# Kernel tuning notes

Hardware: AMD Instinct MI355X
Metric: run time of the kernel (lower is better)

Reference implementation:

```python
import jax, jax.numpy as jnp
import numpy as np

B, N, D, H = 16, 1024, 384, 6
DH = D // H  # 64 per-head dim


def _layernorm(x, w, b, eps=1e-5):
    mu = jnp.mean(x, axis=-1, keepdims=True)
    var = jnp.var(x, axis=-1, keepdims=True)
    return (x - mu) * jax.lax.rsqrt(var + eps) * w + b


def setup_inputs() -> dict:
    key = jax.random.key(0)
    ks = jax.random.split(key, 10)
    std = 0.02
    return {
        "X": jax.random.normal(ks[0], (B, N, D), dtype=jnp.float32),
        "Wq": jax.random.normal(ks[1], (H, DH, D), dtype=jnp.float32) * std,
        "Wk": jax.random.normal(ks[2], (H, DH, D), dtype=jnp.float32) * std,
        "Wv": jax.random.normal(ks[3], (H, DH, D), dtype=jnp.float32) * std,
        "Wo": jax.random.normal(ks[4], (D, D), dtype=jnp.float32) * std,
        "bo": jnp.zeros((D,), dtype=jnp.float32),
        "ln1_w": jnp.ones((D,), dtype=jnp.float32),
        "ln1_b": jnp.zeros((D,), dtype=jnp.float32),
        "ln2_w": jnp.ones((D,), dtype=jnp.float32),
        "ln2_b": jnp.zeros((D,), dtype=jnp.float32),
        "W1": jax.random.normal(ks[5], (2 * D, D), dtype=jnp.float32) * std,
        "b1": jnp.zeros((2 * D,), dtype=jnp.float32),
        "W2": jax.random.normal(ks[6], (D, 2 * D), dtype=jnp.float32) * std,
        "b2": jnp.zeros((D,), dtype=jnp.float32),
    }


def reference(X, Wq, Wk, Wv, Wo, bo, ln1_w, ln1_b, ln2_w, ln2_b, W1, b1, W2, b2):
    scale = 1.0 / jnp.sqrt(jnp.float32(DH))
    # pre-LN then multi-head attention (heads vectorized, math identical to per-head loop)
    t = _layernorm(X, ln1_w, ln1_b)                       # [B,N,D]
    q = jnp.einsum('bnd,hkd->bhnk', t, Wq)                # [B,H,N,DH]
    k = jnp.einsum('bnd,hkd->bhnk', t, Wk)
    v = jnp.einsum('bnd,hkd->bhnk', t, Wv)
    scores = jnp.einsum('bhnk,bhmk->bhnm', q, k) * scale  # [B,H,N,N]
    p = jax.nn.softmax(scores, axis=-1)
    o = jnp.einsum('bhnm,bhmk->bhnk', p, v)               # [B,H,N,DH]
    o = jnp.transpose(o, (0, 2, 1, 3)).reshape(B, N, D)   # concat heads
    attn = o @ Wo.T + bo
    # residual + post-LN (dropout/drop_path are identity in eval)
    X2 = _layernorm(X + attn, ln2_w, ln2_b)
    # MLP: Linear -> exact GELU -> Linear
    h = jax.nn.gelu(X2 @ W1.T + b1, approximate=False)
    mlp = h @ W2.T + b2
    return X2 + mlp
```

## Files before the change

### kernel.cpp

```cpp
#include <hip/hip_runtime.h>
#include <math.h>

typedef float  f32x4  __attribute__((ext_vector_type(4)));
typedef __bf16 bf16x8 __attribute__((ext_vector_type(8)));
typedef __bf16 bf16x4 __attribute__((ext_vector_type(4)));

__device__ __forceinline__ void gload16(const void* g, void* l) {
  __builtin_amdgcn_global_load_lds((__attribute__((address_space(1))) const void*)g,
                                   (__attribute__((address_space(3))) void*)l, 16, 0, 0);
}

__device__ __forceinline__ f32x4 mfma16(bf16x8 a, bf16x8 b, f32x4 c) {
  return __builtin_amdgcn_mfma_f32_16x16x32_bf16(a, b, c, 0, 0, 0);
}

__device__ __forceinline__ f32x4 mfma8(long a, long b, f32x4 c) {
  return __builtin_amdgcn_mfma_f32_16x16x32_fp8_fp8(a, b, c, 0, 0, 0);
}

__device__ __forceinline__ unsigned char f2fp8(float x) {
  return (unsigned char)__builtin_amdgcn_cvt_pk_fp8_f32(x, x, 0, false);
}

__device__ __forceinline__ float fast_gelu(float x) {
  const float xs = x * 0.70710678118654752f;
  const float ax = fabsf(xs);
  const float t  = __builtin_amdgcn_rcpf(1.f + 0.3275911f * ax);
  const float poly = ((((1.061405429f*t - 1.453152027f)*t + 1.421413741f)*t
                       - 0.284496736f)*t + 0.254829592f)*t;
  const float e = __builtin_amdgcn_exp2f(-1.4426950408889634f * ax * ax);
  float erfv = 1.f - poly * e;
  erfv = (xs < 0.f) ? -erfv : erfv;
  return 0.5f * x * (1.f + erfv);
}

__global__ __launch_bounds__(256) void prep_kernel(
    const float* __restrict__ X, const float* __restrict__ ln1w, const float* __restrict__ ln1b,
    unsigned char* __restrict__ t8,
    const float* __restrict__ Wq, const float* __restrict__ Wk, const float* __restrict__ Wv,
    const float* __restrict__ Wo, const float* __restrict__ W1, const float* __restrict__ W2,
    unsigned char* __restrict__ wqkv8, unsigned char* __restrict__ wo8,
    unsigned char* __restrict__ w18, unsigned char* __restrict__ w28)
{
  if (blockIdx.x >= 4096) {
    const int idx = ((blockIdx.x - 4096) * 256 + threadIdx.x) * 4;
    const float* src; unsigned char* dst; int off;
    if      (idx < 147456) { src = Wq; dst = wqkv8;          off = idx; }
    else if (idx < 294912) { src = Wk; dst = wqkv8 + 147456; off = idx - 147456; }
    else if (idx < 442368) { src = Wv; dst = wqkv8 + 294912; off = idx - 294912; }
    else if (idx < 589824) { src = Wo; dst = wo8;            off = idx - 442368; }
    else if (idx < 884736) { src = W1; dst = w18;            off = idx - 589824; }
    else                   { src = W2; dst = w28;            off = idx - 884736; }
    f32x4 v = *(const f32x4*)(src + off);
    int p = __builtin_amdgcn_cvt_pk_fp8_f32(v.x, v.y, 0, false);
    p     = __builtin_amdgcn_cvt_pk_fp8_f32(v.z, v.w, p, true);
    *(int*)(dst + off) = p;
    return;
  }
  const int row  = blockIdx.x * 4 + (threadIdx.x >> 6);
  const int lane = threadIdx.x & 63;
  const float* x = X + (size_t)row * 384;
  float v[6]; float s = 0.f;
#pragma unroll
  for (int j = 0; j < 6; ++j) { v[j] = x[lane + 64*j]; s += v[j]; }
#pragma unroll
  for (int off = 32; off > 0; off >>= 1) s += __shfl_xor(s, off);
  const float mu = s * (1.f/384.f);
  float s2 = 0.f;
#pragma unroll
  for (int j = 0; j < 6; ++j) { float d = v[j] - mu; s2 += d*d; }
#pragma unroll
  for (int off = 32; off > 0; off >>= 1) s2 += __shfl_xor(s2, off);
  const float inv = rsqrtf(s2 * (1.f/384.f) + 1e-5f);
#pragma unroll
  for (int j = 0; j < 6; ++j) {
    const int cidx = lane + 64*j;
    t8[(size_t)row*384 + cidx] = f2fp8((v[j]-mu)*inv*ln1w[cidx] + ln1b[cidx]);
  }
}

__global__ __launch_bounds__(256) void ln_kernel(
    const float* __restrict__ in, const float* __restrict__ w, const float* __restrict__ b,
    unsigned char* __restrict__ outc, float* __restrict__ outf)
{
  const int row  = blockIdx.x * 4 + (threadIdx.x >> 6);
  const int lane = threadIdx.x & 63;
  const float* x = in + (size_t)row * 384;
  float v[6]; float s = 0.f;
#pragma unroll
  for (int j = 0; j < 6; ++j) { v[j] = x[lane + 64*j]; s += v[j]; }
#pragma unroll
  for (int off = 32; off > 0; off >>= 1) s += __shfl_xor(s, off);
  const float mu = s * (1.f/384.f);
  float s2 = 0.f;
#pragma unroll
  for (int j = 0; j < 6; ++j) { float d = v[j] - mu; s2 += d*d; }
#pragma unroll
  for (int off = 32; off > 0; off >>= 1) s2 += __shfl_xor(s2, off);
  const float inv = rsqrtf(s2 * (1.f/384.f) + 1e-5f);
#pragma unroll
  for (int j = 0; j < 6; ++j) {
    const int cidx = lane + 64*j;
    const float y = (v[j]-mu)*inv*w[cidx] + b[cidx];
    outc[(size_t)row*384 + cidx] = f2fp8(y);
    outf[(size_t)row*384 + cidx] = y;
  }
}

template<int EPI>
__global__ __launch_bounds__(256, 3) void gemm_f8(
    const unsigned char* __restrict__ A, const unsigned char* __restrict__ Bw,
    int N, int K,
    const float* __restrict__ bias, const float* __restrict__ resid,
    float* __restrict__ outf, unsigned char* __restrict__ outc,
    __bf16* __restrict__ q_out, __bf16* __restrict__ k_out, __bf16* __restrict__ vt_out)
{
  __shared__ __attribute__((aligned(16))) unsigned char As[2][8192];
  __shared__ __attribute__((aligned(16))) unsigned char Bs[2][8192];
  const int tid  = threadIdx.x;
  const int lane = tid & 63;
  const int w    = tid >> 6;
  const int wm   = w >> 1, wn = w & 1;
  const int m0   = blockIdx.x * 128, n0 = blockIdx.y * 128;

  f32x4 acc[4][4] = {};

  const int srow = lane & 15, skq = (lane >> 4) << 4;
  const unsigned char* gptr[4];
  unsigned char*       lptr[4];
#pragma unroll
  for (int r = 0; r < 4; ++r) {
    const int id = r * 4 + w;
    if (id < 8) { gptr[r] = A  + (size_t)(m0 + id*16 + srow) * K + skq; lptr[r] = &As[0][id * 1024]; }
    else        { const int j = id - 8;
                  gptr[r] = Bw + (size_t)(n0 + j*16 + srow) * K + skq; lptr[r] = &Bs[0][j * 1024]; }
  }

  auto stage = [&](int kk, int b) {
#pragma unroll
    for (int r = 0; r < 4; ++r)
      gload16(gptr[r] + kk * 64, lptr[r] + b * 8192);
  };
  const int lo = lane & 15, quad = lane >> 4;
  const int foff = (quad >> 1) * 256 + lo * 16 + (quad & 1) * 8;
  auto compute = [&](int b) {
#pragma unroll
    for (int s = 0; s < 2; ++s) {
      long af[4], bfr[4];
#pragma unroll
      for (int i = 0; i < 4; ++i)
        af[i]  = *(const long*)&As[b][(wm*4 + i) * 1024 + s * 512 + foff];
#pragma unroll
      for (int j = 0; j < 4; ++j)
        bfr[j] = *(const long*)&Bs[b][(wn*4 + j) * 1024 + s * 512 + foff];
#pragma unroll
      for (int i = 0; i < 4; ++i)
#pragma unroll
        for (int j = 0; j < 4; ++j)
          acc[i][j] = mfma8(af[i], bfr[j], acc[i][j]);
    }
  };

  const int NIT = K >> 6;
  stage(0, 0);
  __syncthreads();
  for (int k = 0; k < NIT; ++k) {
    const int b = k & 1;
    if (k + 1 < NIT) stage(k + 1, b ^ 1);
    compute(b);
    __syncthreads();
  }

#pragma unroll
  for (int rt = 0; rt < 4; ++rt) {
#pragma unroll
    for (int ct = 0; ct < 4; ++ct) {
      const int gr0 = m0 + (wm*4 + rt)*16 + quad*4;
      const int gc  = n0 + (wn*4 + ct)*16 + lo;
      f32x4 a = acc[rt][ct];
      if constexpr (EPI == 0) {
        const int bb = gr0 >> 10, nn = gr0 & 1023;
        if (gc >= 768) {
          const int jj = gc - 768, hh = jj >> 6, dh = jj & 63;
          bf16x4 pk = {(__bf16)a[0], (__bf16)a[1], (__bf16)a[2], (__bf16)a[3]};
          *(bf16x4*)&vt_out[((size_t)((bb*6 + hh)*64 + dh) << 10) + nn] = pk;
        } else {
          const bool isq = (gc < 384);
          const int jj = isq ? gc : (gc - 384);
          __bf16* dst = isq ? q_out : k_out;
          const float sc = isq ? 0.18033688011112042f : 1.0f;
          const int hh = jj >> 6, dh = jj & 63;
#pragma unroll
          for (int i = 0; i < 4; ++i)
            dst[((size_t)(((bb*6 + hh) << 10) | (nn + i)) << 6) + dh] = (__bf16)(a[i] * sc);
        }
      } else {
#pragma unroll
        for (int i = 0; i < 4; ++i) {
          const int gr = gr0 + i;
          float val = a[i];
          if constexpr (EPI == 1) {
            const size_t idx = (size_t)gr * N + gc;
            outf[idx] = val + bias[gc] + resid[idx];
          } else if constexpr (EPI == 2) {
            outc[(size_t)gr * N + gc] = f2fp8(fast_gelu(val + bias[gc]));
          } else {
            const size_t idx = (size_t)gr * N + gc;
            outf[idx] = outf[idx] + val + bias[gc];
          }
        }
      }
    }
  }
}

__global__ __launch_bounds__(256, 3) void attn_kernel(
    const __bf16* __restrict__ qp, const __bf16* __restrict__ kp,
    const __bf16* __restrict__ vtp, unsigned char* __restrict__ omat8)
{
  __shared__ __attribute__((aligned(16))) __bf16 Ks[3][4096];
  __shared__ __attribute__((aligned(16))) __bf16 Vs[2][4096];
  __shared__ __attribute__((aligned(16))) __bf16 Ps[4][1088];
  const int tid = threadIdx.x, lane = tid & 63, w = tid >> 6;
  const int bh = blockIdx.x;
  const int q0 = blockIdx.y * 128 + w * 32;
  const int quad = lane >> 4, lo = lane & 15;

  bf16x8 qa[2][2];
#pragma unroll
  for (int t = 0; t < 2; ++t) {
    const __bf16* qb = qp + ((size_t)bh * 1024 + q0 + t*16 + lo) * 64 + (quad << 3);
    qa[t][0] = *(const bf16x8*)qb;
    qa[t][1] = *(const bf16x8*)(qb + 32);
  }

  f32x4 oacc[2][4] = {};
  float l_r[2] = {0.f, 0.f};

  auto stageK = [&](int c, int kb) {
#pragma unroll
    for (int s = 0; s < 2; ++s) {
      const int ck = s * 256 + tid;
      const int l = ck & 63, g = ck >> 6;
      const int ct = g >> 1, ks = g & 1;
      const __bf16* gk = kp + ((size_t)bh*1024 + c*64 + ct*16 + (l & 15)) * 64
                            + ks*32 + ((l >> 4) << 3);
      gload16(gk, &Ks[kb][(ck & ~63) * 8]);
    }
  };
  auto stageV = [&](int c, int vb) {
#pragma unroll
    for (int s = 0; s < 2; ++s) {
      const int ck = s * 256 + tid;
      const int l = ck & 63, g = ck >> 6;
      const int ct = g >> 1, ks = g & 1;
      const __bf16* gv = vtp + (((size_t)(bh*64 + ct*16 + (l & 15))) << 10)
                             + c*64 + ks*32 + ((l >> 4) << 3);
      gload16(gv, &Vs[vb][(ck & ~63) * 8]);
    }
  };

  stageK(0, 0); stageK(1, 1); stageV(0, 0);
  asm volatile("s_waitcnt vmcnt(0)" ::: "memory");
  __builtin_amdgcn_s_barrier();

  for (int c = 0; c < 16; ++c) {
    const int kb = c % 3;
    const int vb = c & 1;
    if (c + 2 < 16) stageK(c + 2, (c + 2) % 3);
    if (c + 1 < 16) stageV(c + 1, (c + 1) & 1);

    f32x4 st[2][4];
#pragma unroll
    for (int ct = 0; ct < 4; ++ct) {
      bf16x8 kb0 = *(const bf16x8*)&Ks[kb][((ct*2 + 0)*64 + lane) * 8];
      bf16x8 kb1 = *(const bf16x8*)&Ks[kb][((ct*2 + 1)*64 + lane) * 8];
#pragma unroll
      for (int t = 0; t < 2; ++t) {
        f32x4 s0 = {};
        s0 = mfma16(kb0, qa[t][0], s0);
        s0 = mfma16(kb1, qa[t][1], s0);
        st[t][ct] = s0;
      }
    }
    bf16x8 pa[2][2];
#pragma unroll
    for (int t = 0; t < 2; ++t) {
#pragma unroll
      for (int ct = 0; ct < 4; ++ct) {
        const float p0 = __builtin_amdgcn_exp2f(st[t][ct][0]);
        const float p1 = __builtin_amdgcn_exp2f(st[t][ct][1]);
        const float p2 = __builtin_amdgcn_exp2f(st[t][ct][2]);
        const float p3 = __builtin_amdgcn_exp2f(st[t][ct][3]);
        l_r[t] += (p0 + p1) + (p2 + p3);
        bf16x4 pk = {(__bf16)p0, (__bf16)p1, (__bf16)p2, (__bf16)p3};
        *(bf16x4*)&Ps[w][lo*68 + ct*16 + quad*4] = pk;
      }
#pragma unroll
      for (int ks = 0; ks < 2; ++ks)
        pa[t][ks] = *(const bf16x8*)&Ps[w][lo*68 + ks*32 + (quad << 3)];
    }

    if (c <= 13)      asm volatile("s_waitcnt vmcnt(4)" ::: "memory");
    else if (c == 14) asm volatile("s_waitcnt vmcnt(2)" ::: "memory");
    else              asm volatile("s_waitcnt vmcnt(0)" ::: "memory");
    __builtin_amdgcn_sched_barrier(0);
    __builtin_amdgcn_s_barrier();

#pragma unroll
    for (int dt = 0; dt < 4; ++dt)
#pragma unroll
      for (int ks = 0; ks < 2; ++ks) {
        bf16x8 vbv = *(const bf16x8*)&Vs[vb][((dt*2 + ks)*64 + lane) * 8];
#pragma unroll
        for (int t = 0; t < 2; ++t)
          oacc[t][dt] = mfma16(pa[t][ks], vbv, oacc[t][dt]);
      }

    __builtin_amdgcn_s_barrier();
  }

  const int b = bh / 6, h = bh - (bh / 6) * 6;
#pragma unroll
  for (int t = 0; t < 2; ++t) {
    float ls = l_r[t];
    ls += __shfl_xor(ls, 16);
    ls += __shfl_xor(ls, 32);
#pragma unroll
    for (int i = 0; i < 4; ++i) {
      const float linv = 1.f / __shfl(ls, quad*4 + i);
      const int n = q0 + t*16 + quad*4 + i;
#pragma unroll
      for (int dt = 0; dt < 4; ++dt)
        omat8[((size_t)((b << 10) | n)) * 384 + (h << 6) + dt*16 + lo] =
            f2fp8(oacc[t][dt][i] * linv);
    }
  }
}

extern "C" void kernel_launch(void* const* d_in, const int* in_sizes, int n_in,
                              void* d_out, int out_size, void* d_ws, size_t ws_size,
                              hipStream_t stream)
{
  const float* X    = (const float*)d_in[0];
  const float* Wq   = (const float*)d_in[1];
  const float* Wk   = (const float*)d_in[2];
  const float* Wv   = (const float*)d_in[3];
  const float* Wo   = (const float*)d_in[4];
  const float* bo   = (const float*)d_in[5];
  const float* ln1w = (const float*)d_in[6];
  const float* ln1b = (const float*)d_in[7];
  const float* ln2w = (const float*)d_in[8];
  const float* ln2b = (const float*)d_in[9];
  const float* W1   = (const float*)d_in[10];
  const float* b1   = (const float*)d_in[11];
  const float* W2   = (const float*)d_in[12];
  const float* b2   = (const float*)d_in[13];

  char* ws = (char*)d_ws;
  unsigned char* t8   = (unsigned char*)(ws + 0);
  unsigned char* x2_f8 = (unsigned char*)(ws + 6291456);
  __bf16* q_bf  = (__bf16*)(ws + 12582912);
  __bf16* k_bf  = (__bf16*)(ws + 25165824);
  unsigned char* omat8 = (unsigned char*)(ws + 37748736);
  __bf16* vt_bf = (__bf16*)(ws + 50331648);
  float*  s1    = (float*) (ws + 62914560);
  unsigned char* h8 = (unsigned char*)(ws + 62914560);
  unsigned char* wqkv8 = (unsigned char*)(ws + 88080384);
  unsigned char* wo8 = (unsigned char*)(ws + 88522752);
  unsigned char* w18 = (unsigned char*)(ws + 88670208);
  unsigned char* w28 = (unsigned char*)(ws + 88965120);
  float*  out   = (float*)d_out;

  prep_kernel<<<5248, 256, 0, stream>>>(X, ln1w, ln1b, t8,
      Wq, Wk, Wv, Wo, W1, W2, wqkv8, wo8, w18, w28);
  gemm_f8<0><<<dim3(128,9), 256, 0, stream>>>(t8, wqkv8, 1152, 384,
      nullptr, nullptr, nullptr, nullptr, q_bf, k_bf, vt_bf);
  attn_kernel<<<dim3(96,8), 256, 0, stream>>>(q_bf, k_bf, vt_bf, omat8);
  gemm_f8<1><<<dim3(128,3), 256, 0, stream>>>(omat8, wo8, 384, 384,
      bo, X, s1, nullptr, nullptr, nullptr, nullptr);
  ln_kernel<<<4096, 256, 0, stream>>>(s1, ln2w, ln2b, x2_f8, out);
  gemm_f8<2><<<dim3(128,6), 256, 0, stream>>>(x2_f8, w18, 768, 384,
      b1, nullptr, nullptr, h8, nullptr, nullptr, nullptr);
  gemm_f8<3><<<dim3(128,3), 256, 0, stream>>>(h8, w28, 384, 768,
      b2, nullptr, out, nullptr, nullptr, nullptr, nullptr);
}
```

Before: 238.4 us.

## Load V tiles straight into registers and drop the V LDS buffer

The attention kernel no longer stages V chunks through a double-buffered LDS array. Each wave now loads its V fragments directly from global memory into registers, issued right after the score MFMAs and before the next K prefetch. This removes the mid-iteration barrier and its explicit vmcnt waits, and frees LDS so the launch bound can rise from 3 to 4 blocks per CU. The cost is that all four waves in a block fetch the same V tile, which multiplies global/L2 traffic for V. It also leans on in-order vmcnt completion and the end-of-iteration barrier to keep the K buffer reads safe.

```diff
diff --git a/kernel.cpp b/kernel.cpp
--- a/kernel.cpp
+++ b/kernel.cpp
@@ -214,12 +214,11 @@
   }
 }
 
-__global__ __launch_bounds__(256, 3) void attn_kernel(
+__global__ __launch_bounds__(256, 4) void attn_kernel(
     const __bf16* __restrict__ qp, const __bf16* __restrict__ kp,
     const __bf16* __restrict__ vtp, unsigned char* __restrict__ omat8)
 {
   __shared__ __attribute__((aligned(16))) __bf16 Ks[3][4096];
-  __shared__ __attribute__((aligned(16))) __bf16 Vs[2][4096];
   __shared__ __attribute__((aligned(16))) __bf16 Ps[4][1088];
   const int tid = threadIdx.x, lane = tid & 63, w = tid >> 6;
   const int bh = blockIdx.x;
@@ -237,7 +236,7 @@
   f32x4 oacc[2][4] = {};
   float l_r[2] = {0.f, 0.f};
 
-  auto stageK = [&](int c, int kb) {
+  auto stageK = [&](int c, int b) {
 #pragma unroll
     for (int s = 0; s < 2; ++s) {
       const int ck = s * 256 + tid;
@@ -245,36 +244,26 @@
       const int ct = g >> 1, ks = g & 1;
       const __bf16* gk = kp + ((size_t)bh*1024 + c*64 + ct*16 + (l & 15)) * 64
                             + ks*32 + ((l >> 4) << 3);
-      gload16(gk, &Ks[kb][(ck & ~63) * 8]);
+      gload16(gk, &Ks[b][(ck & ~63) * 8]);
     }
   };
-  auto stageV = [&](int c, int vb) {
-#pragma unroll
-    for (int s = 0; s < 2; ++s) {
-      const int ck = s * 256 + tid;
-      const int l = ck & 63, g = ck >> 6;
-      const int ct = g >> 1, ks = g & 1;
-      const __bf16* gv = vtp + (((size_t)(bh*64 + ct*16 + (l & 15))) << 10)
-                             + c*64 + ks*32 + ((l >> 4) << 3);
-      gload16(gv, &Vs[vb][(ck & ~63) * 8]);
-    }
-  };
-
-  stageK(0, 0); stageK(1, 1); stageV(0, 0);
-  asm volatile("s_waitcnt vmcnt(0)" ::: "memory");
+
+  const __bf16* vbase = vtp + (((size_t)(bh*64 + lo)) << 10) + (quad << 3);
+
+  stageK(0, 0); stageK(1, 1);
+  asm volatile("s_waitcnt vmcnt(2)" ::: "memory");
+  __builtin_amdgcn_sched_barrier(0);
   __builtin_amdgcn_s_barrier();
 
+  int rb = 0;
   for (int c = 0; c < 16; ++c) {
-    const int kb = c % 3;
-    const int vb = c & 1;
-    if (c + 2 < 16) stageK(c + 2, (c + 2) % 3);
-    if (c + 1 < 16) stageV(c + 1, (c + 1) & 1);
+    const int sb = (rb == 0) ? 2 : rb - 1;
 
     f32x4 st[2][4];
 #pragma unroll
     for (int ct = 0; ct < 4; ++ct) {
-      bf16x8 kb0 = *(const bf16x8*)&Ks[kb][((ct*2 + 0)*64 + lane) * 8];
-      bf16x8 kb1 = *(const bf16x8*)&Ks[kb][((ct*2 + 1)*64 + lane) * 8];
+      bf16x8 kb0 = *(const bf16x8*)&Ks[rb][((ct*2 + 0)*64 + lane) * 8];
+      bf16x8 kb1 = *(const bf16x8*)&Ks[rb][((ct*2 + 1)*64 + lane) * 8];
 #pragma unroll
       for (int t = 0; t < 2; ++t) {
         f32x4 s0 = {};
@@ -283,6 +272,17 @@
         st[t][ct] = s0;
       }
     }
+
+    bf16x8 vr[4][2];
+#pragma unroll
+    for (int dt = 0; dt < 4; ++dt)
+#pragma unroll
+      for (int ks = 0; ks < 2; ++ks)
+        vr[dt][ks] = *(const bf16x8*)(vbase + ((size_t)dt << 14) + c*64 + ks*32);
+    __builtin_amdgcn_sched_barrier(0);
+    if (c + 2 < 16) stageK(c + 2, sb);
+    __builtin_amdgcn_sched_barrier(0);
+
     bf16x8 pa[2][2];
 #pragma unroll
     for (int t = 0; t < 2; ++t) {
@@ -301,23 +301,17 @@
         pa[t][ks] = *(const bf16x8*)&Ps[w][lo*68 + ks*32 + (quad << 3)];
     }
 
-    if (c <= 13)      asm volatile("s_waitcnt vmcnt(4)" ::: "memory");
-    else if (c == 14) asm volatile("s_waitcnt vmcnt(2)" ::: "memory");
-    else              asm volatile("s_waitcnt vmcnt(0)" ::: "memory");
-    __builtin_amdgcn_sched_barrier(0);
-    __builtin_amdgcn_s_barrier();
-
 #pragma unroll
     for (int dt = 0; dt < 4; ++dt)
 #pragma unroll
       for (int ks = 0; ks < 2; ++ks) {
-        bf16x8 vbv = *(const bf16x8*)&Vs[vb][((dt*2 + ks)*64 + lane) * 8];
 #pragma unroll
         for (int t = 0; t < 2; ++t)
-          oacc[t][dt] = mfma16(pa[t][ks], vbv, oacc[t][dt]);
+          oacc[t][dt] = mfma16(pa[t][ks], vr[dt][ks], oacc[t][dt]);
       }
 
-    __builtin_amdgcn_s_barrier();
+    if (c + 1 < 16) __builtin_amdgcn_s_barrier();
+    rb = (rb == 2) ? 0 : rb + 1;
   }
 
   const int b = bh / 6, h = bh - (bh / 6) * 6;
```

After: 294.2 us. +23.4%, slower.
